# Kernel tuning notes

Measured on AMD Instinct MI355X. Metric: run time of the kernel, lower is better.

Reference implementation:

```python
import jax, jax.numpy as jnp
import numpy as np

B, N = 4096, 8192

def setup_inputs() -> dict:
    key = jax.random.key(0)
    k1, k2, k3 = jax.random.split(key, 3)
    y_pred = jax.random.normal(k1, (B, N), dtype=jnp.float32)
    y_true = jax.random.normal(k2, (B, N), dtype=jnp.float32)
    x_values = jnp.arange(N, dtype=jnp.float32)  # monotone strain grid
    fracture_idx = jax.random.randint(k3, (B,), 0, N)  # per-sample fracture point
    return {"y_pred": y_pred, "y_true": y_true, "x_values": x_values,
            "fracture_idx": fracture_idx}

def _masked_trapz(y, x_values, fracture_idx):
    # trapezoid areas of every segment: [B, N-1]
    dx = x_values[1:] - x_values[:-1]                       # [N-1]
    seg = 0.5 * (y[:, :-1] + y[:, 1:]) * dx[None, :]        # [B, N-1]
    # segment j contributes iff j+1 <= fracture_idx, i.e. j < fracture_idx
    npts = y.shape[1]
    mask = jnp.arange(npts - 1)[None, :] < fracture_idx[:, None]
    return jnp.sum(jnp.where(mask, seg, 0.0), axis=1)       # [B]

def reference(y_pred, y_true, x_values, fracture_idx):
    # fracture_idx clamped to valid range as in torch module
    idx = jnp.clip(fracture_idx, 0, y_pred.shape[1] - 1)
    pred_int = _masked_trapz(y_pred, x_values, idx)
    true_int = _masked_trapz(y_true, x_values, idx)
    err_sq = (pred_int - true_int) ** 2                     # [B]
    return jnp.mean(err_sq)  # reduction='mean'
```

## Files before the change

### kernel.cpp

```cpp
#include <hip/hip_runtime.h>
#include <hip/hip_bf16.h>

__global__ __launch_bounds__(256) void strain_loss_kernel(
    const float* __restrict__ y_pred,
    const float* __restrict__ y_true,
    const float* __restrict__ x,
    const int*   __restrict__ fidx,
    float* __restrict__ out,
    int n, float inv_b)
{
    const int row = blockIdx.x;
    const int tid = threadIdx.x;

    int idx = fidx[row];
    idx = idx < 0 ? 0 : (idx > n - 1 ? n - 1 : idx);

    const float* p = y_pred + (long long)row * n;
    const float* t = y_true + (long long)row * n;

    float acc = 0.0f;
    for (int k0 = tid * 4; k0 <= idx; k0 += 256 * 4) {
        float4 pv = *(const float4*)(p + k0);
        float4 tv = *(const float4*)(t + k0);
        float4 xv = *(const float4*)(x + k0);
        float xm = (k0 >= 1)     ? x[k0 - 1] : xv.x;
        float xp = (k0 + 4 < n)  ? x[k0 + 4] : xv.w;
        float xs[6] = {xm, xv.x, xv.y, xv.z, xv.w, xp};
        float dv[4] = {pv.x - tv.x, pv.y - tv.y, pv.z - tv.z, pv.w - tv.w};
        #pragma unroll
        for (int e = 0; e < 4; ++e) {
            int k = k0 + e;
            float left  = (k >= 1 && k <= idx) ? (xs[e + 1] - xs[e])     : 0.0f;
            float right = (k < idx)            ? (xs[e + 2] - xs[e + 1]) : 0.0f;
            acc += 0.5f * (left + right) * dv[e];
        }
    }

    #pragma unroll
    for (int off = 32; off > 0; off >>= 1)
        acc += __shfl_down(acc, off, 64);

    __shared__ float wave_sums[4];
    const int wave = tid >> 6;
    if ((tid & 63) == 0) wave_sums[wave] = acc;
    __syncthreads();

    if (tid == 0) {
        float s = wave_sums[0] + wave_sums[1] + wave_sums[2] + wave_sums[3];
        atomicAdd(out, s * s * inv_b);
    }
}

extern "C" void kernel_launch(void* const* d_in, const int* in_sizes, int n_in,
                              void* d_out, int out_size, void* d_ws, size_t ws_size,
                              hipStream_t stream) {
    const float* y_pred = (const float*)d_in[0];
    const float* y_true = (const float*)d_in[1];
    const float* x      = (const float*)d_in[2];
    const int*   fidx   = (const int*)d_in[3];
    float* out = (float*)d_out;

    const int n = in_sizes[2];
    const int b = in_sizes[3];

    hipMemsetAsync(d_out, 0, sizeof(float), stream);

    strain_loss_kernel<<<dim3(b), dim3(256), 0, stream>>>(
        y_pred, y_true, x, fidx, out, n, 1.0f / (float)b);
}
```

Measured before the change: 263.6 us.

## Split rows into chunks across a 2D grid with a separate finalize reduction

Each row is now processed by several blocks, one per 1024-element chunk, and each block writes its partial sum to workspace. Blocks whose chunk starts past the fracture index exit early. A single-block finalize kernel sums the chunks per row, squares, and averages, which replaces the global atomicAdd and the memset. The aim is to balance the uneven per-row work caused by the random fracture indices and raise parallelism, at the cost of a second launch and a serial finalize over 4096 rows.

```diff
diff --git a/kernel.cpp b/kernel.cpp
--- a/kernel.cpp
+++ b/kernel.cpp
@@ -1,30 +1,42 @@
 #include <hip/hip_runtime.h>
-#include <hip/hip_bf16.h>
 
-__global__ __launch_bounds__(256) void strain_loss_kernel(
+
+#define CHUNK 1024
+
+__global__ __launch_bounds__(256) void strain_partial_kernel(
     const float* __restrict__ y_pred,
     const float* __restrict__ y_true,
     const float* __restrict__ x,
     const int*   __restrict__ fidx,
-    float* __restrict__ out,
-    int n, float inv_b)
+    float* __restrict__ ws,
+    int n)
 {
-    const int row = blockIdx.x;
-    const int tid = threadIdx.x;
+    const int row    = blockIdx.x;
+    const int chunk  = blockIdx.y;
+    const int nchunk = gridDim.y;
+    const int tid    = threadIdx.x;
 
     int idx = fidx[row];
     idx = idx < 0 ? 0 : (idx > n - 1 ? n - 1 : idx);
 
-    const float* p = y_pred + (long long)row * n;
-    const float* t = y_true + (long long)row * n;
+    const int base = chunk * CHUNK;
+    const long long slot = (long long)row * nchunk + chunk;
+
+    if (base > idx) {
+        if (tid == 0) ws[slot] = 0.0f;
+        return;
+    }
 
     float acc = 0.0f;
-    for (int k0 = tid * 4; k0 <= idx; k0 += 256 * 4) {
+    const int k0 = base + tid * 4;
+    if (k0 <= idx) {
+        const float* p = y_pred + (long long)row * n;
+        const float* t = y_true + (long long)row * n;
         float4 pv = *(const float4*)(p + k0);
         float4 tv = *(const float4*)(t + k0);
         float4 xv = *(const float4*)(x + k0);
-        float xm = (k0 >= 1)     ? x[k0 - 1] : xv.x;
-        float xp = (k0 + 4 < n)  ? x[k0 + 4] : xv.w;
+        float xm = (k0 >= 1)    ? x[k0 - 1] : xv.x;
+        float xp = (k0 + 4 < n) ? x[k0 + 4] : xv.w;
         float xs[6] = {xm, xv.x, xv.y, xv.z, xv.w, xp};
         float dv[4] = {pv.x - tv.x, pv.y - tv.y, pv.z - tv.z, pv.w - tv.w};
         #pragma unroll
@@ -41,13 +53,53 @@
         acc += __shfl_down(acc, off, 64);
 
     __shared__ float wave_sums[4];
-    const int wave = tid >> 6;
-    if ((tid & 63) == 0) wave_sums[wave] = acc;
+    if ((tid & 63) == 0) wave_sums[tid >> 6] = acc;
+    __syncthreads();
+
+    if (tid == 0)
+        ws[slot] = wave_sums[0] + wave_sums[1] + wave_sums[2] + wave_sums[3];
+}
+
+__global__ __launch_bounds__(1024) void strain_finalize_kernel(
+    const float* __restrict__ ws,
+    float* __restrict__ out,
+    int b, int nchunk, float inv_b)
+{
+    const int tid = threadIdx.x;
+    float acc = 0.0f;
+
+    if ((nchunk & 3) == 0) {
+        for (int r = tid; r < b; r += 1024) {
+            const float4* w = (const float4*)(ws + (long long)r * nchunk);
+            float s = 0.0f;
+            for (int c = 0; c < (nchunk >> 2); ++c) {
+                float4 v = w[c];
+                s += (v.x + v.y) + (v.z + v.w);
+            }
+            acc += s * s;
+        }
+    } else {
+        for (int r = tid; r < b; r += 1024) {
+            float s = 0.0f;
+            for (int c = 0; c < nchunk; ++c)
+                s += ws[(long long)r * nchunk + c];
+            acc += s * s;
+        }
+    }
+
+    #pragma unroll
+    for (int off = 32; off > 0; off >>= 1)
+        acc += __shfl_down(acc, off, 64);
+
+    __shared__ float wave_sums[16];
+    if ((tid & 63) == 0) wave_sums[tid >> 6] = acc;
     __syncthreads();
 
     if (tid == 0) {
-        float s = wave_sums[0] + wave_sums[1] + wave_sums[2] + wave_sums[3];
-        atomicAdd(out, s * s * inv_b);
+        float s = 0.0f;
+        #pragma unroll
+        for (int w = 0; w < 16; ++w) s += wave_sums[w];
+        out[0] = s * inv_b;
     }
 }
 
@@ -59,12 +111,14 @@
     const float* x      = (const float*)d_in[2];
     const int*   fidx   = (const int*)d_in[3];
     float* out = (float*)d_out;
+    float* ws  = (float*)d_ws;
 
     const int n = in_sizes[2];
     const int b = in_sizes[3];
+    const int nchunk = (n + CHUNK - 1) / CHUNK;
 
-    hipMemsetAsync(d_out, 0, sizeof(float), stream);
-
-    strain_loss_kernel<<<dim3(b), dim3(256), 0, stream>>>(
-        y_pred, y_true, x, fidx, out, n, 1.0f / (float)b);
+    strain_partial_kernel<<<dim3(b, nchunk), dim3(256), 0, stream>>>(
+        y_pred, y_true, x, fidx, ws, n);
+    strain_finalize_kernel<<<dim3(1), dim3(1024), 0, stream>>>(
+        ws, out, b, nchunk, 1.0f / (float)b);
 }
```

Result: faster. 252.4 us (-4.2%).
